# Performance work log

Hardware: AMD Instinct MI355X
Metric: run time of the kernel (lower is better)

Reference implementation:

```python
import jax, jax.numpy as jnp
import numpy as np

GAMMA = 0.25
GN_EPS = 1e-5


def setup_inputs() -> dict:
    key = jax.random.key(0)
    k1, k2, k3 = jax.random.split(key, 3)
    B, T, C = 16, 2048, 512
    G, V, Dv = 2, 320, 256
    x = jax.random.normal(k1, (B, T, C), dtype=jnp.float32)
    conv_w = jax.random.normal(k2, (G, C // G, C // G), dtype=jnp.float32) * 0.05
    gn_w = jnp.ones((C,), dtype=jnp.float32)
    gn_b = jnp.zeros((C,), dtype=jnp.float32)
    emb = 0.01 * jax.random.normal(k3, (V, G, Dv), dtype=jnp.float32)
    return {"x": x, "conv_w": conv_w, "gn_w": gn_w, "gn_b": gn_b, "emb": emb}


def _vq_forward(x, conv_w, gn_w, gn_b, emb):
    B, T, C = x.shape
    V, G, Dv = emb.shape
    sg = jax.lax.stop_gradient
    # time_first -> BxCxT
    xt = jnp.transpose(x, (0, 2, 1))  # [B,C,T]
    # grouped 1x1 conv (no bias)
    xg = xt.reshape(B, G, C // G, T)
    ze = jnp.einsum('goi,bgit->bgot', conv_w, xg)  # [B,G,C/G,T]
    # Fp32GroupNorm over (C/G, T) per group, biased variance
    zf = ze.astype(jnp.float32)
    mu = jnp.mean(zf, axis=(2, 3), keepdims=True)
    var = jnp.mean(jnp.square(zf - mu), axis=(2, 3), keepdims=True)
    zn = ((zf - mu) * jax.lax.rsqrt(var + GN_EPS)).reshape(B, C, T)
    ze = (zn * gn_w[None, :, None] + gn_b[None, :, None]).astype(ze.dtype)  # [B,C,T]
    # split into groups along feature dim: [B,T,G,Dv]
    ze_ = jnp.transpose(ze.reshape(B, G, Dv, T), (0, 3, 1, 2))
    # squared distances [V,B,T,G] (argmin of ||.||_2 == argmin of ||.||_2^2)
    d2 = (jnp.sum(jnp.square(ze_), axis=-1)[None]
          - 2.0 * jnp.einsum('btgd,vgd->vbtg', ze_, emb)
          + jnp.sum(jnp.square(emb), axis=-1)[:, None, None, :])
    idx = jnp.argmin(d2, axis=0)  # [B,T,G] int
    # gather nearest codewords per group
    zq = emb[idx, jnp.arange(G)[None, None, :]]  # [B,T,G,Dv]
    zq = jnp.transpose(zq.reshape(B, T, C), (0, 2, 1))  # [B,C,T]
    # straight-through
    out = sg(zq) + (ze - sg(ze))  # [B,C,T]
    # code perplexity (no grad)
    probs = jnp.mean(jax.nn.one_hot(sg(idx), V, dtype=jnp.float32), axis=(0, 1))  # [G,V]
    perplexity = jnp.sum(jnp.exp(-jnp.sum(probs * jnp.log(probs + 1e-7), axis=-1)))
    # losses
    zef, zqf = ze.astype(jnp.float32), zq.astype(jnp.float32)
    latent = jnp.mean(jnp.square(zqf - sg(zef)))
    commit = jnp.mean(jnp.square(zef - sg(zqf)))
    loss = latent + GAMMA * commit
    out = jnp.transpose(out, (0, 2, 1))  # back to BxTxC
    return out, loss, perplexity, idx


def reference(x, conv_w, gn_w, gn_b, emb):
    return _vq_forward(x, conv_w, gn_w, gn_b, emb)
```

## Files before the change

kernel.cpp:

```cpp
#include <hip/hip_runtime.h>

#define Bq 16
#define Tq 2048
#define Cq 512
#define Gq 2
#define CGq 256
#define Vq 320
#define Mq 32768
#define LOSS_OFF 16777216
#define PPL_OFF  16777217
#define IDX_OFF  16777218

#define MARGIN 1.75e-4f
#define LIST_CAP 16384
#define LIST2_CAP 1024

#define WS_PCONV 0
#define WS_PLOSS 16384
#define WS_MU    49152
#define WS_RS    49280
#define WS_E2    49408
#define WS_LOSSF 51968
#define WS_CNT   51976
#define WS_CNT2  51980
#define WS_HIST  51984
#define WS_PL2   54544
#define WS_LIST2 70928
#define WS_WSP   131072
#define WS_LISTQ 917504

typedef short s16x8 __attribute__((ext_vector_type(8)));
typedef float f32x4v __attribute__((ext_vector_type(4)));

__device__ __forceinline__ void bsplit(float x, unsigned &b1, unsigned &b2) {
    unsigned u = __float_as_uint(x);
    unsigned r1 = (u + 0x7fffu + ((u >> 16) & 1u)) & 0xffff0000u;
    b1 = r1 >> 16;
    float d = x - __uint_as_float(r1);
    unsigned u2 = __float_as_uint(d);
    b2 = (u2 + 0x7fffu + ((u2 >> 16) & 1u)) >> 16;
}

__device__ __forceinline__ void bsplit3(float x, unsigned &h, unsigned &m, unsigned &l) {
    unsigned u = __float_as_uint(x);
    unsigned r1 = (u + 0x7fffu + ((u >> 16) & 1u)) & 0xffff0000u;
    h = r1 >> 16;
    float d1 = x - __uint_as_float(r1);
    unsigned u2 = __float_as_uint(d1);
    unsigned r2 = (u2 + 0x7fffu + ((u2 >> 16) & 1u)) & 0xffff0000u;
    m = r2 >> 16;
    float d2 = d1 - __uint_as_float(r2);
    unsigned u3 = __float_as_uint(d2);
    l = (u3 + 0x7fffu + ((u3 >> 16) & 1u)) >> 16;
}

__global__ __launch_bounds__(256) void k_e2(const float* __restrict__ emb,
                                            float* __restrict__ e2w) {
    int row  = blockIdx.x * 4 + (threadIdx.x >> 6);
    int lane = threadIdx.x & 63;
    float4 v = *(const float4*)(emb + (size_t)row * 256 + lane * 4);
    float s = v.x * v.x + v.y * v.y + v.z * v.z + v.w * v.w;
#pragma unroll
    for (int m = 1; m < 64; m <<= 1) s += __shfl_xor(s, m);
    if (lane == 0) e2w[(row & 1) * Vq + (row >> 1)] = s;
}

__global__ __launch_bounds__(256) void k_wsplit(const float* __restrict__ w,
                                                unsigned char* __restrict__ wsp) {
    int t = blockIdx.x * 256 + threadIdx.x;
    int g = t >> 13, o = (t >> 5) & 255, ihi = t & 31;
    const float* src = w + ((size_t)(g * 256 + o)) * 256 + ihi * 8;
    float xv[8];
    *(float4*)(xv + 0) = *(const float4*)(src);
    *(float4*)(xv + 4) = *(const float4*)(src + 4);
    unsigned ph[4] = {0,0,0,0}, pm[4] = {0,0,0,0}, pl[4] = {0,0,0,0};
#pragma unroll
    for (int e = 0; e < 8; e++) {
        unsigned h, m, l;
        bsplit3(xv[e], h, m, l);
        ph[e >> 1] |= h << ((e & 1) * 16);
        pm[e >> 1] |= m << ((e & 1) * 16);
        pl[e >> 1] |= l << ((e & 1) * 16);
    }
    int kc = ihi >> 2, quad = ihi & 3, ct = o >> 4, lf = o & 15;
    size_t base = (size_t)(g * 3) * 131072 + (size_t)kc * 16384 + ct * 1024 + quad * 256 + lf * 16;
    *(uint4*)(wsp + base + 0 * 131072) = *(uint4*)ph;
    *(uint4*)(wsp + base + 1 * 131072) = *(uint4*)pm;
    *(uint4*)(wsp + base + 2 * 131072) = *(uint4*)pl;
}

__global__ __launch_bounds__(256, 2) void k_convM(const float* __restrict__ x,
    const unsigned char* __restrict__ wsp, float* __restrict__ ze,
    double* __restrict__ pconv)
{
    __shared__ unsigned char lds[73728];
    __shared__ double reds[4], redq[4];
    uint4* Bs = (uint4*)lds;
    uint4* As = (uint4*)(lds + 49152);

    int tid = threadIdx.x, bx = blockIdx.x;
    int mt = bx >> 1, g = bx & 1;
    int m0 = mt * 128;
    int w = tid >> 6, lane = tid & 63;
    int quad = lane >> 4, l15 = lane & 15;
    int arow = tid >> 1, ah = tid & 1;
    int aw = arow >> 5, art = (arow >> 4) & 1, ar = arow & 15;
    const float* xrow = x + (size_t)(m0 + arow) * Cq + g * CGq + ah * 16;
    const unsigned char* wslab = wsp + (size_t)(g * 3) * 131072;

    f32x4v zero4 = {0.f, 0.f, 0.f, 0.f};
    f32x4v acc[2][16];
#pragma unroll
    for (int i = 0; i < 2; i++)
#pragma unroll
        for (int j = 0; j < 16; j++) acc[i][j] = zero4;

    for (int kc = 0; kc < 8; kc++) {
        if (kc) __syncthreads();
#pragma unroll
        for (int j = 0; j < 12; j++) {
            int L = (w * 12 + j) * 1024 + lane * 16;
            int p = L >> 14, r = L & 16383;
            __builtin_amdgcn_global_load_lds(
                (const __attribute__((address_space(1))) void*)(wslab + (size_t)p * 131072 + (size_t)kc * 16384 + r),
                (__attribute__((address_space(3))) void*)(lds + L), 16, 0, 0);
        }
        float xv[16];
        *(float4*)(xv + 0)  = *(const float4*)(xrow + kc * 32 + 0);
        *(float4*)(xv + 4)  = *(const float4*)(xrow + kc * 32 + 4);
        *(float4*)(xv + 8)  = *(const float4*)(xrow + kc * 32 + 8);
        *(float4*)(xv + 12) = *(const float4*)(xrow + kc * 32 + 12);
#pragma unroll
        for (int ii = 0; ii < 2; ii++) {
            unsigned ph[4] = {0,0,0,0}, pm[4] = {0,0,0,0}, pl[4] = {0,0,0,0};
#pragma unroll
            for (int e = 0; e < 8; e++) {
                unsigned h, m, l;
                bsplit3(xv[ii * 8 + e], h, m, l);
                ph[e >> 1] |= h << ((e & 1) * 16);
                pm[e >> 1] |= m << ((e & 1) * 16);
                pl[e >> 1] |= l << ((e & 1) * 16);
            }
            int aq = ah * 2 + ii;
            As[(((0 * 4 + aw) * 2 + art) * 4 + aq) * 16 + ar] = *(uint4*)ph;
            As[(((1 * 4 + aw) * 2 + art) * 4 + aq) * 16 + ar] = *(uint4*)pm;
            As[(((2 * 4 + aw) * 2 + art) * 4 + aq) * 16 + ar] = *(uint4*)pl;
        }
        __syncthreads();
        s16x8 afr[3][2];
#pragma unroll
        for (int p = 0; p < 3; p++)
#pragma unroll
            for (int rt = 0; rt < 2; rt++)
                afr[p][rt] = __builtin_bit_cast(s16x8,
                    As[(((p * 4 + w) * 2 + rt) * 4 + quad) * 16 + l15]);
#pragma unroll
        for (int ct = 0; ct < 16; ct++) {
            s16x8 b0 = __builtin_bit_cast(s16x8, Bs[0 * 1024 + ct * 64 + quad * 16 + l15]);
            s16x8 b1 = __builtin_bit_cast(s16x8, Bs[1 * 1024 + ct * 64 + quad * 16 + l15]);
            s16x8 b2 = __builtin_bit_cast(s16x8, Bs[2 * 1024 + ct * 64 + quad * 16 + l15]);
#pragma unroll
            for (int rt = 0; rt < 2; rt++) {
                acc[rt][ct] = __builtin_amdgcn_mfma_f32_16x16x32_bf16(afr[0][rt], b0, acc[rt][ct], 0, 0, 0);
                acc[rt][ct] = __builtin_amdgcn_mfma_f32_16x16x32_bf16(afr[1][rt], b0, acc[rt][ct], 0, 0, 0);
                acc[rt][ct] = __builtin_amdgcn_mfma_f32_16x16x32_bf16(afr[2][rt], b0, acc[rt][ct], 0, 0, 0);
                acc[rt][ct] = __builtin_amdgcn_mfma_f32_16x16x32_bf16(afr[0][rt], b1, acc[rt][ct], 0, 0, 0);
                acc[rt][ct] = __builtin_amdgcn_mfma_f32_16x16x32_bf16(afr[1][rt], b1, acc[rt][ct], 0, 0, 0);
                acc[rt][ct] = __builtin_amdgcn_mfma_f32_16x16x32_bf16(afr[0][rt], b2, acc[rt][ct], 0, 0, 0);
            }
        }
    }

    float s = 0.f, q = 0.f;
    float* zb = ze + (size_t)m0 * Cq + g * CGq;
#pragma unroll
    for (int rt = 0; rt < 2; rt++)
#pragma unroll
    for (int ct = 0; ct < 16; ct++)
#pragma unroll
    for (int j = 0; j < 4; j++) {
        float v = acc[rt][ct][j];
        zb[(size_t)(w * 32 + rt * 16 + quad * 4 + j) * Cq + ct * 16 + l15] = v;
        s += v;
        q = __builtin_fmaf(v, v, q);
    }
    double ds = (double)s, dq = (double)q;
#pragma unroll
    for (int m = 1; m < 64; m <<= 1) { ds += __shfl_xor(ds, m); dq += __shfl_xor(dq, m); }
    if (lane == 0) { reds[w] = ds; redq[w] = dq; }
    __syncthreads();
    if (tid == 0) {
        pconv[bx * 2 + 0] = reds[0] + reds[1] + reds[2] + reds[3];
        pconv[bx * 2 + 1] = redq[0] + redq[1] + redq[2] + redq[3];
    }
}

__global__ __launch_bounds__(256) void k_stats(const double* __restrict__ pconv,
                                               float* __restrict__ muw,
                                               float* __restrict__ rsw) {
    int tid = threadIdx.x;
    int bg = tid >> 3, r = tid & 7;
    int b = bg >> 1, g = bg & 1;
    double s = 0.0, q = 0.0;
    for (int j = r; j < 16; j += 8) {
        int pi = (b * 16 + j) * 2 + g;
        s += pconv[pi * 2 + 0];
        q += pconv[pi * 2 + 1];
    }
#pragma unroll
    for (int m = 1; m < 8; m <<= 1) { s += __shfl_xor(s, m); q += __shfl_xor(q, m); }
    if (r == 0) {
        double mu = s / 524288.0;
        double var = q / 524288.0 - mu * mu;
        double rs = 1.0 / sqrt(var + 1e-5);
        muw[bg] = (float)mu;
        rsw[bg] = (float)rs;
    }
}

__global__ __launch_bounds__(256, 2) void k_distA(const float* __restrict__ emb,
    const float* __restrict__ gw, const float* __restrict__ gb,
    const float* __restrict__ muw, const float* __restrict__ rsw,
    const float* __restrict__ e2w, float* dout,
    unsigned* __restrict__ cntw, unsigned* __restrict__ cnt2w,
    unsigned long long* __restrict__ listq, unsigned* __restrict__ list2)
{
    __shared__ uint4 Asl[1024];
    __shared__ uint4 Bsl[2560];
    __shared__ float e2s[Vq];

    int tid = threadIdx.x, bx = blockIdx.x;
    int mt = bx >> 1, g = bx & 1;
    int m0 = mt * 128;
    int bg = (m0 >> 11) * 2 + g;
    float muf = muw[bg], rsf = rsw[bg];
    int w = tid >> 6, lane = tid & 63;
    int quad = lane >> 4, l15 = lane & 15;

    for (int i = tid; i < Vq; i += 256) e2s[i] = e2w[g * Vq + i];

    int arow = tid >> 1, ah = tid & 1;
    int aw = arow >> 5, art = (arow >> 4) & 1, ar = arow & 15;
    const float* zrow = dout + (size_t)m0 * Cq + g * CGq + (size_t)arow * Cq;
    int bv = tid >> 3, bk4 = (tid & 7) * 4;

    f32x4v zero4 = {0.f, 0.f, 0.f, 0.f};
    f32x4v acc[2][20];
#pragma unroll
    for (int i = 0; i < 2; i++)
#pragma unroll
        for (int j = 0; j < 20; j++) acc[i][j] = zero4;

    for (int kc8 = 0; kc8 < 8; kc8++) {
        if (kc8) __syncthreads();
        int k0 = kc8 * 32;
#pragma unroll
        for (int i2 = 0; i2 < 2; i2++) {
            uint4 o1, o2;
            unsigned hw[4], lw[4];
#pragma unroll
            for (int ii = 0; ii < 2; ii++) {
                int koff = k0 + ah * 16 + i2 * 8 + ii * 4;
                float4 z  = *(const float4*)(zrow + koff);
                float4 gv = *(const float4*)(gw + g * CGq + koff);
                float4 bvv= *(const float4*)(gb + g * CGq + koff);
                float zn0 = (z.x - muf) * rsf * gv.x + bvv.x;
                float zn1 = (z.y - muf) * rsf * gv.y + bvv.y;
                float zn2 = (z.z - muf) * rsf * gv.z + bvv.z;
                float zn3 = (z.w - muf) * rsf * gv.w + bvv.w;
                unsigned h0,l0,h1,l1,h2,l2,h3,l3;
                bsplit(zn0, h0, l0); bsplit(zn1, h1, l1);
                bsplit(zn2, h2, l2); bsplit(zn3, h3, l3);
                hw[ii*2+0] = h0 | (h1 << 16); hw[ii*2+1] = h2 | (h3 << 16);
                lw[ii*2+0] = l0 | (l1 << 16); lw[ii*2+1] = l2 | (l3 << 16);
            }
            o1.x = hw[0]; o1.y = hw[1]; o1.z = hw[2]; o1.w = hw[3];
            o2.x = lw[0]; o2.y = lw[1]; o2.z = lw[2]; o2.w = lw[3];
            int kq = ah * 2 + i2;
            Asl[(((0*4 + aw)*2 + art)*4 + kq)*16 + ar] = o1;
            Asl[(((1*4 + aw)*2 + art)*4 + kq)*16 + ar] = o2;
        }
#pragma unroll
        for (int r = 0; r < 10; r++) {
            int v = r * 32 + bv;
            float4 e4 = *(const float4*)(emb + ((size_t)v * Gq + g) * CGq + k0 + bk4);
            unsigned h0,l0,h1,l1,h2,l2,h3,l3;
            bsplit(e4.x, h0, l0); bsplit(e4.y, h1, l1);
            bsplit(e4.z, h2, l2); bsplit(e4.w, h3, l3);
            uint2 hv; hv.x = h0 | (h1 << 16); hv.y = h2 | (h3 << 16);
            uint2 lv; lv.x = l0 | (l1 << 16); lv.y = l2 | (l3 << 16);
            int half = (bk4 >> 2) & 1;
            int s0 = ((0*20 + (v >> 4))*4 + (bk4 >> 3))*16 + (v & 15);
            int s1 = ((1*20 + (v >> 4))*4 + (bk4 >> 3))*16 + (v & 15);
            ((uint2*)&Bsl[s0])[half] = hv;
            ((uint2*)&Bsl[s1])[half] = lv;
        }
        __syncthreads();
        s16x8 afr[2][2];
#pragma unroll
        for (int s = 0; s < 2; s++)
#pragma unroll
            for (int rt = 0; rt < 2; rt++)
                afr[s][rt] = __builtin_bit_cast(s16x8,
                    Asl[(((s*4 + w)*2 + rt)*4 + quad)*16 + l15]);
#pragma unroll
        for (int ct = 0; ct < 20; ct++) {
            s16x8 b0 = __builtin_bit_cast(s16x8, Bsl[((0*20 + ct)*4 + quad)*16 + l15]);
            s16x8 b1 = __builtin_bit_cast(s16x8, Bsl[((1*20 + ct)*4 + quad)*16 + l15]);
#pragma unroll
            for (int rt = 0; rt < 2; rt++) {
                acc[rt][ct] = __builtin_amdgcn_mfma_f32_16x16x32_bf16(afr[0][rt], b0, acc[rt][ct], 0, 0, 0);
                acc[rt][ct] = __builtin_amdgcn_mfma_f32_16x16x32_bf16(afr[0][rt], b1, acc[rt][ct], 0, 0, 0);
                acc[rt][ct] = __builtin_amdgcn_mfma_f32_16x16x32_bf16(afr[1][rt], b0, acc[rt][ct], 0, 0, 0);
            }
        }
    }

#pragma unroll
    for (int rt = 0; rt < 2; rt++)
#pragma unroll
    for (int j = 0; j < 4; j++) {
        float m1 = 3.402823466e+38f; int i1 = 0;
#pragma unroll
        for (int ct = 0; ct < 20; ct++) {
            float d2a = e2s[ct * 16 + l15] - 2.0f * acc[rt][ct][j];
            if (d2a < m1) { m1 = d2a; i1 = ct * 16 + l15; }
        }
#pragma unroll
        for (int mm = 1; mm < 16; mm <<= 1) {
            float ov = __shfl_xor(m1, mm);
            int   oi = __shfl_xor(i1, mm);
            if (ov < m1 || (ov == m1 && oi < i1)) { m1 = ov; i1 = oi; }
        }
        float thr = m1 + MARGIN;
        unsigned mask = 0;
#pragma unroll
        for (int ct = 0; ct < 20; ct++) {
            float d2a = e2s[ct * 16 + l15] - 2.0f * acc[rt][ct][j];
            if (d2a <= thr) mask |= (1u << ct);
        }
        int cnt = __popc(mask);
#pragma unroll
        for (int mm = 1; mm < 16; mm <<= 1) cnt += __shfl_xor(cnt, mm);
        int mrow = m0 + w * 32 + rt * 16 + quad * 4 + j;
        unsigned q = (unsigned)mrow * 2u + (unsigned)g;
        unsigned flag = 0;
        if (cnt > 1) {
            if ((i1 & 15) == l15) mask &= ~(1u << (i1 >> 4));
            int cl2 = __popc(mask);
            int inc = cl2;
#pragma unroll
            for (int off = 1; off < 16; off <<= 1) {
                int t = __shfl_up(inc, off, 16);
                if (l15 >= off) inc += t;
            }
            int pre = inc - cl2;
            if (cnt <= 5) {
                int pos_ = 0;
                if (l15 == 0) pos_ = (int)atomicAdd(cntw, 1u);
                pos_ = __shfl(pos_, 0, 16);
                if ((unsigned)pos_ < LIST_CAP) {
                    flag = 512u;
                    unsigned long long contrib = 0ull;
                    unsigned mm2 = mask; int k = pre;
                    while (mm2) {
                        int ct2 = __ffs(mm2) - 1; mm2 &= mm2 - 1;
                        contrib |= ((unsigned long long)(unsigned)(ct2 * 16 + l15)) << (20 + 9 * k);
                        k++;
                    }
#pragma unroll
                    for (int mm = 1; mm < 16; mm <<= 1)
                        contrib |= __shfl_xor(contrib, mm);
                    if (l15 == 0)
                        listq[pos_] = (unsigned long long)q
                                    | ((unsigned long long)(unsigned)cnt << 17) | contrib;
                }
            } else {
                if (l15 == 0) {
                    unsigned p2 = atomicAdd(cnt2w, 1u);
                    if (p2 < LIST2_CAP) { list2[p2] = q; flag = 512u; }
                }
            }
        }
        if (l15 == 0) dout[IDX_OFF + q] = __uint_as_float((unsigned)i1 | flag);
    }
}

__global__ __launch_bounds__(256) void k_exS(const float* __restrict__ emb,
    const float* __restrict__ gw, const float* __restrict__ gb,
    const float* __restrict__ muw, const float* __restrict__ rsw,
    const float* __restrict__ e2w, float* dout,
    unsigned* __restrict__ hist, double* __restrict__ ploss)
{
    int tid = threadIdx.x;
    int lane = tid & 63;
    int wid = blockIdx.x * 4 + (tid >> 6);
    int quad = lane >> 2, j = lane & 3;
    int q = wid * 16 + quad;
    int m = q >> 1, g = q & 1;
    int bg = (m >> 11) * 2 + g;
    float muf = muw[bg], rsf = rsw[bg];
    unsigned packed = __float_as_uint(dout[IDX_OFF + q]);
    int flag = (packed >> 9) & 1;
    int v = packed & 511;
    const float* zb  = dout + (size_t)m * Cq + g * CGq;
    const float* gwb = gw + g * CGq;
    const float* gbb = gb + g * CGq;
    const float* eb  = emb + ((size_t)v * Gq + g) * CGq;
    float z2p = 0.f, dp = 0.f;
    for (int kc = 0; kc < 16; kc++) {
        int k0 = kc * 16 + j * 4;
        float4 z  = *(const float4*)(zb + k0);
        float4 gv = *(const float4*)(gwb + k0);
        float4 bv = *(const float4*)(gbb + k0);
        float4 e4 = *(const float4*)(eb + k0);
        float zn0 = __fadd_rn(__fmul_rn(__fmul_rn(__fsub_rn(z.x, muf), rsf), gv.x), bv.x);
        float zn1 = __fadd_rn(__fmul_rn(__fmul_rn(__fsub_rn(z.y, muf), rsf), gv.y), bv.y);
        float zn2 = __fadd_rn(__fmul_rn(__fmul_rn(__fsub_rn(z.z, muf), rsf), gv.z), bv.z);
        float zn3 = __fadd_rn(__fmul_rn(__fmul_rn(__fsub_rn(z.w, muf), rsf), gv.w), bv.w);
        z2p = __builtin_fmaf(zn0, zn0, z2p);
        z2p = __builtin_fmaf(zn1, zn1, z2p);
        z2p = __builtin_fmaf(zn2, zn2, z2p);
        z2p = __builtin_fmaf(zn3, zn3, z2p);
        dp = __builtin_fmaf(zn0, e4.x, dp);
        dp = __builtin_fmaf(zn1, e4.y, dp);
        dp = __builtin_fmaf(zn2, e4.z, dp);
        dp = __builtin_fmaf(zn3, e4.w, dp);
    }
    z2p += __shfl_xor(z2p, 1); z2p += __shfl_xor(z2p, 2);
    dp  += __shfl_xor(dp, 1);  dp  += __shfl_xor(dp, 2);
    float d2 = __fadd_rn(__fsub_rn(z2p, 2.0f * dp), e2w[g * Vq + v]);
    double lp = 0.0;
    if (!flag && j == 0) {
        dout[IDX_OFF + q] = (float)v;
        atomicAdd(&hist[g * Vq + v], 1u);
        lp = (double)d2;
    }
#pragma unroll
    for (int mm = 1; mm < 64; mm <<= 1) lp += __shfl_xor(lp, mm);
    if (lane == 0) ploss[wid] = lp;
}

__global__ __launch_bounds__(256) void k_exF3(const float* __restrict__ emb,
    const float* __restrict__ gw, const float* __restrict__ gb,
    const float* __restrict__ muw, const float* __restrict__ rsw,
    const float* __restrict__ e2w, float* dout,
    unsigned* __restrict__ hist, double* __restrict__ ploss2,
    const unsigned long long* __restrict__ listq, const unsigned* __restrict__ cntw)
{
    int tid = threadIdx.x, lane = tid & 63;
    int gwid = blockIdx.x * 4 + (tid >> 6);
    int cslot = lane >> 2, j = lane & 3;
    unsigned nn = *cntw; if (nn > LIST_CAP) nn = LIST_CAP;
    int n = (int)nn;
    double lacc = 0.0;
    for (int it = gwid; it < n; it += 2048) {
        unsigned long long e = listq[it];
        unsigned q = (unsigned)(e & 0x1FFFFull);
        int cnt = (int)((e >> 17) & 7u);
        int m = (int)(q >> 1), g = (int)(q & 1u);
        int bg = (m >> 11) * 2 + g;
        float muf = muw[bg], rsf = rsw[bg];
        int v = (int)(__float_as_uint(dout[IDX_OFF + q]) & 511u);
        if (cslot >= 1 && cslot < cnt)
            v = (int)((e >> (20 + 9 * (cslot - 1))) & 511ull);
        const float* zb  = dout + (size_t)m * Cq + g * CGq;
        const float* gwb = gw + g * CGq;
        const float* gbb = gb + g * CGq;
        const float* eb  = emb + ((size_t)v * Gq + g) * CGq;
        float z2p = 0.f, dp = 0.f;
        for (int kc = 0; kc < 16; kc++) {
            int k0 = kc * 16 + j * 4;
            float4 z  = *(const float4*)(zb + k0);
            float4 gv = *(const float4*)(gwb + k0);
            float4 bv = *(const float4*)(gbb + k0);
            float4 e4 = *(const float4*)(eb + k0);
            float zn0 = __fadd_rn(__fmul_rn(__fmul_rn(__fsub_rn(z.x, muf), rsf), gv.x), bv.x);
            float zn1 = __fadd_rn(__fmul_rn(__fmul_rn(__fsub_rn(z.y, muf), rsf), gv.y), bv.y);
            float zn2 = __fadd_rn(__fmul_rn(__fmul_rn(__fsub_rn(z.z, muf), rsf), gv.z), bv.z);
            float zn3 = __fadd_rn(__fmul_rn(__fmul_rn(__fsub_rn(z.w, muf), rsf), gv.w), bv.w);
            z2p = __builtin_fmaf(zn0, zn0, z2p);
            z2p = __builtin_fmaf(zn1, zn1, z2p);
            z2p = __builtin_fmaf(zn2, zn2, z2p);
            z2p = __builtin_fmaf(zn3, zn3, z2p);
            dp = __builtin_fmaf(zn0, e4.x, dp);
            dp = __builtin_fmaf(zn1, e4.y, dp);
            dp = __builtin_fmaf(zn2, e4.z, dp);
            dp = __builtin_fmaf(zn3, e4.w, dp);
        }
        z2p += __shfl_xor(z2p, 1); z2p += __shfl_xor(z2p, 2);
        dp  += __shfl_xor(dp, 1);  dp  += __shfl_xor(dp, 2);
        float d2 = __fadd_rn(__fsub_rn(z2p, 2.0f * dp), e2w[g * Vq + v]);
#pragma unroll
        for (int mm = 4; mm < 64; mm <<= 1) {
            float od = __shfl_xor(d2, mm);
            int   ov = __shfl_xor(v, mm);
            if (od < d2 || (od == d2 && ov < v)) { d2 = od; v = ov; }
        }
        if (lane == 0) {
            dout[IDX_OFF + q] = (float)v;
            atomicAdd(&hist[g * Vq + v], 1u);
            lacc += (double)d2;
        }
    }
    if (lane == 0) ploss2[gwid] = lacc;
}

__global__ __launch_bounds__(256) void k_exFslow(const float* __restrict__ emb,
    const float* __restrict__ gw, const float* __restrict__ gb,
    const float* __restrict__ muw, const float* __restrict__ rsw,
    const float* __restrict__ e2w, float* dout,
    unsigned* __restrict__ hist, double* __restrict__ lossf,
    const unsigned* __restrict__ cnt2w, const unsigned* __restrict__ list2)
{
    int tid = threadIdx.x, lane = tid & 63;
    int wid = blockIdx.x * 4 + (tid >> 6);
    unsigned nn = *cnt2w; if (nn > LIST2_CAP) nn = LIST2_CAP;
    int n = (int)nn;
    for (int it = wid; it < n; it += 128) {
        int q = (int)list2[it];
        int m = q >> 1, g = q & 1;
        int bg = (m >> 11) * 2 + g;
        float muf = muw[bg], rsf = rsw[bg];
        const float* zb = dout + (size_t)m * Cq + g * CGq;
        int k0 = lane * 4;
        float4 z  = *(const float4*)(zb + k0);
        float4 gv = *(const float4*)(gw + g * CGq + k0);
        float4 bv = *(const float4*)(gb + g * CGq + k0);
        float zn0 = __fadd_rn(__fmul_rn(__fmul_rn(__fsub_rn(z.x, muf), rsf), gv.x), bv.x);
        float zn1 = __fadd_rn(__fmul_rn(__fmul_rn(__fsub_rn(z.y, muf), rsf), gv.y), bv.y);
        float zn2 = __fadd_rn(__fmul_rn(__fmul_rn(__fsub_rn(z.z, muf), rsf), gv.z), bv.z);
        float zn3 = __fadd_rn(__fmul_rn(__fmul_rn(__fsub_rn(z.w, muf), rsf), gv.w), bv.w);
        float s = 0.f;
        for (int kc = 0; kc < 16; kc++) {
            int src = (lane & 3) + kc * 4;
            float a0 = __shfl(zn0, src), a1 = __shfl(zn1, src);
            float a2 = __shfl(zn2, src), a3 = __shfl(zn3, src);
            s = __builtin_fmaf(a0, a0, s);
            s = __builtin_fmaf(a1, a1, s);
            s = __builtin_fmaf(a2, a2, s);
            s = __builtin_fmaf(a3, a3, s);
        }
        s += __shfl_xor(s, 1); s += __shfl_xor(s, 2);
        float z2 = s;
        float m1 = 3.402823466e+38f; int i1 = 0;
        for (int v = 0; v < Vq; v += 2) {
            const float* e0 = emb + ((size_t)v * Gq + g) * CGq + k0;
            float4 ea = *(const float4*)e0;
            float4 eb4 = *(const float4*)(e0 + Gq * CGq);
            float da = zn0 * ea.x;  da = __builtin_fmaf(zn1, ea.y, da);
            da = __builtin_fmaf(zn2, ea.z, da); da = __builtin_fmaf(zn3, ea.w, da);
            float db = zn0 * eb4.x; db = __builtin_fmaf(zn1, eb4.y, db);
            db = __builtin_fmaf(zn2, eb4.z, db); db = __builtin_fmaf(zn3, eb4.w, db);
#pragma unroll
            for (int mm = 1; mm < 64; mm <<= 1) { da += __shfl_xor(da, mm); db += __shfl_xor(db, mm); }
            float d2a = __fadd_rn(__fsub_rn(z2, 2.0f * da), e2w[g * Vq + v]);
            float d2b = __fadd_rn(__fsub_rn(z2, 2.0f * db), e2w[g * Vq + v + 1]);
            if (d2a < m1) { m1 = d2a; i1 = v; }
            if (d2b < m1) { m1 = d2b; i1 = v + 1; }
        }
        if (lane == 0) {
            dout[IDX_OFF + q] = (float)i1;
            atomicAdd(&hist[g * Vq + i1], 1u);
            atomicAdd(lossf, (double)m1);
        }
    }
}

__global__ __launch_bounds__(256) void k_out(const float* __restrict__ emb, float* dout) {
    size_t u = (size_t)blockIdx.x * 256 + threadIdx.x;
    size_t pos = u * 4;
    int m = (int)(pos >> 9);
    int c = (int)(pos & 511);
    int g = c >> 8, d = c & 255;
    int v = (int)dout[IDX_OFF + (size_t)m * Gq + g];
    float4 o = *(const float4*)(emb + ((size_t)(v * 2 + g)) * 256 + d);
    *(float4*)(dout + pos) = o;
}

__global__ __launch_bounds__(256) void k_final(const double* __restrict__ ploss,
                                               const double* __restrict__ ploss2,
                                               const double* __restrict__ lossf,
                                               const unsigned* __restrict__ hist,
                                               float* dout) {
    __shared__ double redl[4], red0[4], red1[4];
    int tid = threadIdx.x;
    double s = 0.0;
    for (int i = tid; i < 4096; i += 256) s += ploss[i];
    for (int i = tid; i < 2048; i += 256) s += ploss2[i];
#pragma unroll
    for (int m = 1; m < 64; m <<= 1) s += __shfl_xor(s, m);
    double e0 = 0.0, e1 = 0.0;
    for (int pid = tid; pid < 640; pid += 256) {
        double p = (double)hist[pid] * (1.0 / 32768.0);
        double t = p * log(p + 1e-7);
        if (pid < 320) e0 += t; else e1 += t;
    }
#pragma unroll
    for (int m = 1; m < 64; m <<= 1) { e0 += __shfl_xor(e0, m); e1 += __shfl_xor(e1, m); }
    int lane = tid & 63, wv_ = tid >> 6;
    if (lane == 0) { redl[wv_] = s; red0[wv_] = e0; red1[wv_] = e1; }
    __syncthreads();
    if (tid == 0) {
        double S  = redl[0] + redl[1] + redl[2] + redl[3] + *lossf;
        double E0 = red0[0] + red0[1] + red0[2] + red0[3];
        double E1 = red1[0] + red1[1] + red1[2] + red1[3];
        dout[LOSS_OFF] = (float)(1.25 * S / 16777216.0);
        dout[PPL_OFF]  = (float)(exp(-E0) + exp(-E1));
    }
}

extern "C" void kernel_launch(void* const* d_in, const int* in_sizes, int n_in,
                              void* d_out, int out_size, void* d_ws, size_t ws_size,
                              hipStream_t stream) {
    const float* x   = (const float*)d_in[0];
    const float* w   = (const float*)d_in[1];
    const float* gw  = (const float*)d_in[2];
    const float* gb  = (const float*)d_in[3];
    const float* emb = (const float*)d_in[4];
    float* dout = (float*)d_out;
    char* ws = (char*)d_ws;
    double* pconv   = (double*)(ws + WS_PCONV);
    double* ploss   = (double*)(ws + WS_PLOSS);
    float* muw      = (float*)(ws + WS_MU);
    float* rsw      = (float*)(ws + WS_RS);
    float* e2w      = (float*)(ws + WS_E2);
    double* lossf   = (double*)(ws + WS_LOSSF);
    unsigned* cntw  = (unsigned*)(ws + WS_CNT);
    unsigned* cnt2w = (unsigned*)(ws + WS_CNT2);
    unsigned* hist  = (unsigned*)(ws + WS_HIST);
    double* ploss2  = (double*)(ws + WS_PL2);
    unsigned* list2 = (unsigned*)(ws + WS_LIST2);
    unsigned char* wsp = (unsigned char*)(ws + WS_WSP);
    unsigned long long* listq = (unsigned long long*)(ws + WS_LISTQ);

    hipMemsetAsync(ws + WS_LOSSF, 0, 2576, stream);
    k_e2<<<160, 256, 0, stream>>>(emb, e2w);
    k_wsplit<<<64, 256, 0, stream>>>(w, wsp);
    k_convM<<<512, 256, 0, stream>>>(x, wsp, dout, pconv);
    k_stats<<<1, 256, 0, stream>>>(pconv, muw, rsw);
    k_distA<<<512, 256, 0, stream>>>(emb, gw, gb, muw, rsw, e2w, dout, cntw, cnt2w, listq, list2);
    k_exS<<<1024, 256, 0, stream>>>(emb, gw, gb, muw, rsw, e2w, dout, hist, ploss);
    k_exF3<<<512, 256, 0, stream>>>(emb, gw, gb, muw, rsw, e2w, dout, hist, ploss2, listq, cntw);
    k_exFslow<<<32, 256, 0, stream>>>(emb, gw, gb, muw, rsw, e2w, dout, hist, lossf, cnt2w, list2);
    k_out<<<16384, 256, 0, stream>>>(emb, dout);
    k_final<<<1, 256, 0, stream>>>(ploss, ploss2, lossf, hist, dout);
}
```

Baseline: 179.7 us.

## Pre-split codebook once and stream it into LDS via direct global loads; swizzle A tiles

Measured after the change: 186.1 us. 1.04x slower.

```diff
diff --git a/kernel.cpp b/kernel.cpp
--- a/kernel.cpp
+++ b/kernel.cpp
@@ -29,6 +29,8 @@
 #define WS_WSP   131072
 #define WS_LISTQ 917504
 
+#define SL(X, r) ((X) * 16 + ((r) ^ ((X) & 7)))
+
 typedef short s16x8 __attribute__((ext_vector_type(8)));
 typedef float f32x4v __attribute__((ext_vector_type(4)));
 
@@ -89,6 +91,36 @@
     *(uint4*)(wsp + base + 2 * 131072) = *(uint4*)pl;
 }
 
+__global__ __launch_bounds__(256) void k_esplit(const float* __restrict__ emb,
+                                                unsigned char* __restrict__ esp) {
+    int t = blockIdx.x * 256 + threadIdx.x;
+    int g  = t / 10240;
+    int r  = t - g * 10240;
+    int kc = r / 1280;
+    int r2 = r - kc * 1280;
+    int ct = r2 >> 6;
+    int r3 = r2 & 63;
+    int kq = r3 >> 4, l15 = r3 & 15;
+    int v  = ct * 16 + l15;
+    int k0 = kc * 32 + kq * 8;
+    const float* src = emb + ((size_t)v * 2 + g) * 256 + k0;
+    float xv[8];
+    *(float4*)(xv + 0) = *(const float4*)(src);
+    *(float4*)(xv + 4) = *(const float4*)(src + 4);
+    unsigned ph[4] = {0,0,0,0}, pl[4] = {0,0,0,0};
+#pragma unroll
+    for (int e = 0; e < 8; e++) {
+        unsigned h, l;
+        bsplit(xv[e], h, l);
+        ph[e >> 1] |= h << ((e & 1) * 16);
+        pl[e >> 1] |= l << ((e & 1) * 16);
+    }
+    size_t base = (size_t)g * 327680 + (size_t)kc * 20480
+                + (size_t)((ct * 4 + kq) * 16 + l15) * 16;
+    *(uint4*)(esp + base) = *(uint4*)ph;
+    *(uint4*)(esp + base + 163840) = *(uint4*)pl;
+}
+
 __global__ __launch_bounds__(256, 2) void k_convM(const float* __restrict__ x,
     const unsigned char* __restrict__ wsp, float* __restrict__ ze,
     double* __restrict__ pconv)
@@ -142,9 +174,9 @@
                 pl[e >> 1] |= l << ((e & 1) * 16);
             }
             int aq = ah * 2 + ii;
-            As[(((0 * 4 + aw) * 2 + art) * 4 + aq) * 16 + ar] = *(uint4*)ph;
-            As[(((1 * 4 + aw) * 2 + art) * 4 + aq) * 16 + ar] = *(uint4*)pm;
-            As[(((2 * 4 + aw) * 2 + art) * 4 + aq) * 16 + ar] = *(uint4*)pl;
+            As[SL(((0 * 4 + aw) * 2 + art) * 4 + aq, ar)] = *(uint4*)ph;
+            As[SL(((1 * 4 + aw) * 2 + art) * 4 + aq, ar)] = *(uint4*)pm;
+            As[SL(((2 * 4 + aw) * 2 + art) * 4 + aq, ar)] = *(uint4*)pl;
         }
         __syncthreads();
         s16x8 afr[3][2];
@@ -153,7 +185,7 @@
 #pragma unroll
             for (int rt = 0; rt < 2; rt++)
                 afr[p][rt] = __builtin_bit_cast(s16x8,
-                    As[(((p * 4 + w) * 2 + rt) * 4 + quad) * 16 + l15]);
+                    As[SL(((p * 4 + w) * 2 + rt) * 4 + quad, l15)]);
 #pragma unroll
         for (int ct = 0; ct < 16; ct++) {
             s16x8 b0 = __builtin_bit_cast(s16x8, Bs[0 * 1024 + ct * 64 + quad * 16 + l15]);
@@ -218,7 +250,7 @@
     }
 }
 
-__global__ __launch_bounds__(256, 2) void k_distA(const float* __restrict__ emb,
+__global__ __launch_bounds__(256, 2) void k_distA(const unsigned char* __restrict__ esp,
     const float* __restrict__ gw, const float* __restrict__ gb,
     const float* __restrict__ muw, const float* __restrict__ rsw,
     const float* __restrict__ e2w, float* dout,
@@ -226,8 +258,9 @@
     unsigned long long* __restrict__ listq, unsigned* __restrict__ list2)
 {
     __shared__ uint4 Asl[1024];
-    __shared__ uint4 Bsl[2560];
+    __shared__ unsigned char ldsB[40960];
     __shared__ float e2s[Vq];
+    uint4* Bsl = (uint4*)ldsB;
 
     int tid = threadIdx.x, bx = blockIdx.x;
     int mt = bx >> 1, g = bx & 1;
@@ -242,7 +275,7 @@
     int arow = tid >> 1, ah = tid & 1;
     int aw = arow >> 5, art = (arow >> 4) & 1, ar = arow & 15;
     const float* zrow = dout + (size_t)m0 * Cq + g * CGq + (size_t)arow * Cq;
-    int bv = tid >> 3, bk4 = (tid & 7) * 4;
+    const unsigned char* eslab = esp + (size_t)g * 327680;
 
     f32x4v zero4 = {0.f, 0.f, 0.f, 0.f};
     f32x4v acc[2][20];
@@ -254,6 +287,14 @@
     for (int kc8 = 0; kc8 < 8; kc8++) {
         if (kc8) __syncthreads();
         int k0 = kc8 * 32;
+#pragma unroll
+        for (int j = 0; j < 10; j++) {
+            int L = j * 4096 + tid * 16;
+            int s = (j >= 5) ? 1 : 0;
+            __builtin_amdgcn_global_load_lds(
+                (const __attribute__((address_space(1))) void*)(eslab + (size_t)s * 143360 + (size_t)kc8 * 20480 + L),
+                (__attribute__((address_space(3))) void*)(ldsB + L), 16, 0, 0);
+        }
 #pragma unroll
         for (int i2 = 0; i2 < 2; i2++) {
             uint4 o1, o2;
@@ -277,23 +318,8 @@
             o1.x = hw[0]; o1.y = hw[1]; o1.z = hw[2]; o1.w = hw[3];
             o2.x = lw[0]; o2.y = lw[1]; o2.z = lw[2]; o2.w = lw[3];
             int kq = ah * 2 + i2;
-            Asl[(((0*4 + aw)*2 + art)*4 + kq)*16 + ar] = o1;
-            Asl[(((1*4 + aw)*2 + art)*4 + kq)*16 + ar] = o2;
-        }
-#pragma unroll
-        for (int r = 0; r < 10; r++) {
-            int v = r * 32 + bv;
-            float4 e4 = *(const float4*)(emb + ((size_t)v * Gq + g) * CGq + k0 + bk4);
-            unsigned h0,l0,h1,l1,h2,l2,h3,l3;
-            bsplit(e4.x, h0, l0); bsplit(e4.y, h1, l1);
-            bsplit(e4.z, h2, l2); bsplit(e4.w, h3, l3);
-            uint2 hv; hv.x = h0 | (h1 << 16); hv.y = h2 | (h3 << 16);
-            uint2 lv; lv.x = l0 | (l1 << 16); lv.y = l2 | (l3 << 16);
-            int half = (bk4 >> 2) & 1;
-            int s0 = ((0*20 + (v >> 4))*4 + (bk4 >> 3))*16 + (v & 15);
-            int s1 = ((1*20 + (v >> 4))*4 + (bk4 >> 3))*16 + (v & 15);
-            ((uint2*)&Bsl[s0])[half] = hv;
-            ((uint2*)&Bsl[s1])[half] = lv;
+            Asl[SL(((0*4 + aw)*2 + art)*4 + kq, ar)] = o1;
+            Asl[SL(((1*4 + aw)*2 + art)*4 + kq, ar)] = o2;
         }
         __syncthreads();
         s16x8 afr[2][2];
@@ -302,7 +328,7 @@
 #pragma unroll
             for (int rt = 0; rt < 2; rt++)
                 afr[s][rt] = __builtin_bit_cast(s16x8,
-                    Asl[(((s*4 + w)*2 + rt)*4 + quad)*16 + l15]);
+                    Asl[SL(((s*4 + w)*2 + rt)*4 + quad, l15)]);
 #pragma unroll
         for (int ct = 0; ct < 20; ct++) {
             s16x8 b0 = __builtin_bit_cast(s16x8, Bsl[((0*20 + ct)*4 + quad)*16 + l15]);
@@ -638,8 +664,9 @@
     k_e2<<<160, 256, 0, stream>>>(emb, e2w);
     k_wsplit<<<64, 256, 0, stream>>>(w, wsp);
     k_convM<<<512, 256, 0, stream>>>(x, wsp, dout, pconv);
+    k_esplit<<<80, 256, 0, stream>>>(emb, wsp);
     k_stats<<<1, 256, 0, stream>>>(pconv, muw, rsw);
-    k_distA<<<512, 256, 0, stream>>>(emb, gw, gb, muw, rsw, e2w, dout, cntw, cnt2w, listq, list2);
+    k_distA<<<512, 256, 0, stream>>>(wsp, gw, gb, muw, rsw, e2w, dout, cntw, cnt2w, listq, list2);
     k_exS<<<1024, 256, 0, stream>>>(emb, gw, gb, muw, rsw, e2w, dout, hist, ploss);
     k_exF3<<<512, 256, 0, stream>>>(emb, gw, gb, muw, rsw, e2w, dout, hist, ploss2, listq, cntw);
     k_exFslow<<<32, 256, 0, stream>>>(emb, gw, gb, muw, rsw, e2w, dout, hist, lossf, cnt2w, list2);
```
